# Kernel optimization log

Hardware: AMD Instinct MI355X
Metric: run time of the kernel (lower is better)

Reference implementation:

```python
import jax, jax.numpy as jnp
import numpy as np

B, A, D = 512, 32, 256      # batch clips, actors (nodes per graph), feature dim
E = 1048576                 # total edges over the flattened (B*A)-node graph
THRESHOLD = 0.5             # config.knn.threshold
EPS = 1e-5


def setup_inputs() -> dict:
    key = jax.random.key(0)
    k1, k2, k3 = jax.random.split(key, 3)
    N = B * A
    X = jax.random.normal(k1, (B, A, D), dtype=jnp.float32)
    edge_index = jax.random.randint(k2, (2, E), 0, N, dtype=jnp.int32)
    W = jax.random.normal(k3, (D, D), dtype=jnp.float32) * (1.0 / np.sqrt(D))
    b = jnp.zeros((D,), dtype=jnp.float32)
    return {"X": X, "edge_index": edge_index, "W": W, "b": b}


def gcn_conv(x, edge_index, W, b):
    # Standard GCNConv: x' = D^-1/2 (A + I) D^-1/2 (x W) + b
    N = x.shape[0]
    x = x @ W                                            # [N, D]
    loop = jnp.arange(N, dtype=edge_index.dtype)
    src = jnp.concatenate([edge_index[0], loop])         # message sources
    tgt = jnp.concatenate([edge_index[1], loop])         # aggregation targets
    deg = jax.ops.segment_sum(jnp.ones_like(src, dtype=x.dtype), tgt,
                              num_segments=N)            # in-degree incl. self-loop
    dinv = jnp.where(deg > 0, jax.lax.rsqrt(deg), 0.0)
    coef = (dinv[src] * dinv[tgt])[:, None]              # symmetric norm per edge
    out = jax.ops.segment_sum(x[src] * coef, tgt, num_segments=N)
    return out + b


def reference(X, edge_index, W, b):
    Bq, Aq, Dq = X.shape
    x = X.reshape(Bq * Aq, Dq)
    x = gcn_conv(x, edge_index, W, b)
    Xo = x.reshape(Bq, Aq, Dq)

    # cal_edge: pairwise squared distances per batch, min-max normalized,
    # thresholded. Instead of variable-length dense_to_sparse edge lists we
    # return the equivalent fixed-shape adjacency mask [B, A, A].
    inner = -2.0 * jnp.einsum('bad,bcd->bac', Xo, Xo)
    sq = jnp.sum(Xo * Xo, axis=-1, keepdims=True)        # [B, A, 1]
    scores = sq + inner + jnp.swapaxes(sq, -1, -2)       # [B, A, A]
    smin = scores.min(axis=-1, keepdims=True)
    smax = scores.max(axis=-1, keepdims=True)
    scores = (scores - smin) / (smax - smin + EPS)
    adj_mask = scores > THRESHOLD                        # new edge set (dense form)
    return Xo, adj_mask
```

## Files before the change

kernel.cpp:

```cpp
#include <hip/hip_runtime.h>

#define BQ 512
#define AQ 32
#define DQ 256
#define NQ (BQ * AQ)
#define EQ 1048576
#define THR 0.5f
#define EPSF 1e-5f
#define DEG_STRIDE 160
#define BIN_TGTS 64
#define NBINS (NQ / BIN_TGTS)
#define BIN_STRIDE 4864
#define HD 128

typedef __attribute__((ext_vector_type(8))) short bf16x8;
typedef __attribute__((ext_vector_type(4))) float f32x4;

__device__ __forceinline__ unsigned short f2bf(float f) {
    unsigned int u = __float_as_uint(f);
    return (unsigned short)((u + 0x7FFFu + ((u >> 16) & 1u)) >> 16);
}
__device__ __forceinline__ float bf2f(unsigned short h) {
    return __uint_as_float((unsigned int)h << 16);
}

__global__ __launch_bounds__(256) void k_prep_part(
        const float* __restrict__ W, unsigned short* __restrict__ Wt,
        const int* __restrict__ src, const int* __restrict__ tgt,
        int* __restrict__ bin_cursor, unsigned int* __restrict__ binned) {
    __shared__ int hist[NBINS];
    int tid = threadIdx.x;
    if (blockIdx.x < 256) {
        int idx = blockIdx.x * 256 + tid;
        int n = idx >> 8;
        int k = idx & 255;
        float w = W[k * DQ + n];
        unsigned short h = f2bf(w);
        Wt[idx] = h;
        Wt[DQ * DQ + idx] = f2bf(w - bf2f(h));
        return;
    }
    hist[tid] = 0;
    __syncthreads();
    int base = (blockIdx.x - 256) * 4096;
    int t[16], s[16];
    #pragma unroll
    for (int i = 0; i < 16; i++) {
        int e = base + i * 256 + tid;
        t[i] = tgt[e];
        s[i] = src[e];
        atomicAdd(&hist[t[i] >> 6], 1);
    }
    __syncthreads();
    int mine = hist[tid];
    __syncthreads();
    hist[tid] = tid * BIN_STRIDE + atomicAdd(&bin_cursor[tid], mine);
    __syncthreads();
    #pragma unroll
    for (int i = 0; i < 16; i++) {
        int slot = atomicAdd(&hist[t[i] >> 6], 1);
        binned[slot] = ((unsigned int)t[i] << 14) | (unsigned int)s[i];
    }
}

__global__ __launch_bounds__(256) void k_bucket_gemm(
        const float* __restrict__ Xp, const unsigned short* __restrict__ Wt,
        unsigned short* __restrict__ xwb,
        const int* __restrict__ bin_cursor, const unsigned int* __restrict__ binned,
        unsigned short* __restrict__ bucket, int* __restrict__ cnt) {
    __shared__ unsigned short lbuck[BIN_TGTS * DEG_STRIDE];
    __shared__ int lcnt[BIN_TGTS];
    int tid = threadIdx.x;
    if (blockIdx.x < NBINS) {
        int b = blockIdx.x;
        if (tid < BIN_TGTS) lcnt[tid] = 0;
        __syncthreads();
        int beg = b * BIN_STRIDE;
        int count = bin_cursor[b];
        if (count > BIN_STRIDE) count = BIN_STRIDE;
        int end = beg + count;
        for (int i = beg + tid; i < end; i += 256) {
            unsigned int ed = binned[i];
            int tl = (int)(ed >> 14) & 63;
            int pos = atomicAdd(&lcnt[tl], 1);
            if (pos < DEG_STRIDE)
                lbuck[tl * DEG_STRIDE + pos] = (unsigned short)(ed & 0x3FFFu);
        }
        __syncthreads();
        const unsigned int* lb32 = (const unsigned int*)lbuck;
        unsigned int* gb32 = (unsigned int*)(bucket + (size_t)b * BIN_TGTS * DEG_STRIDE);
        #pragma unroll
        for (int i = 0; i < 20; i++) gb32[i * 256 + tid] = lb32[i * 256 + tid];
        if (tid < BIN_TGTS) cnt[b * BIN_TGTS + tid] = lcnt[tid];
        return;
    }
    int wave = tid >> 6;
    int lane = tid & 63;
    int col = lane & 15;
    int quad = lane >> 4;
    int mbase = (blockIdx.x - NBINS) * 64 + wave * 16;
    int m = mbase + col;

    const float* arow = Xp + (size_t)m * DQ;
    const unsigned short* Wlo = Wt + DQ * DQ;

    f32x4 acc[16];
    f32x4 zero = {0.f, 0.f, 0.f, 0.f};
    #pragma unroll
    for (int i = 0; i < 16; i++) acc[i] = zero;

    for (int k0 = 0; k0 < DQ; k0 += 32) {
        int kq = k0 + quad * 8;
        float4 a0 = *(const float4*)(arow + kq);
        float4 a1 = *(const float4*)(arow + kq + 4);
        float av[8] = {a0.x, a0.y, a0.z, a0.w, a1.x, a1.y, a1.z, a1.w};
        bf16x8 ah, al;
        #pragma unroll
        for (int j = 0; j < 8; j++) {
            unsigned short h = f2bf(av[j]);
            ah[j] = (short)h;
            al[j] = (short)f2bf(av[j] - bf2f(h));
        }
        #pragma unroll
        for (int nt = 0; nt < 16; nt++) {
            size_t boff = (size_t)(nt * 16 + col) * DQ + kq;
            bf16x8 bh = *(const bf16x8*)(Wt + boff);
            bf16x8 bl = *(const bf16x8*)(Wlo + boff);
            acc[nt] = __builtin_amdgcn_mfma_f32_16x16x32_bf16(ah, bh, acc[nt], 0, 0, 0);
            acc[nt] = __builtin_amdgcn_mfma_f32_16x16x32_bf16(al, bh, acc[nt], 0, 0, 0);
            acc[nt] = __builtin_amdgcn_mfma_f32_16x16x32_bf16(ah, bl, acc[nt], 0, 0, 0);
        }
    }

    #pragma unroll
    for (int nt = 0; nt < 16; nt++) {
        int gc = nt * 16 + col;
        unsigned short* dst = xwb + (size_t)(gc >> 7) * NQ * HD;
        int c = gc & (HD - 1);
        #pragma unroll
        for (int r = 0; r < 4; r++) {
            dst[(size_t)(mbase + quad * 4 + r) * HD + c] = f2bf(acc[nt][r]);
        }
    }
}

__global__ __launch_bounds__(256) void k_agg(const unsigned int* __restrict__ xwb,
                                             const int* __restrict__ cnt,
                                             const unsigned short* __restrict__ bucket,
                                             const float* __restrict__ bias,
                                             float* __restrict__ out) {
    int wave = threadIdx.x >> 6;
    int lane = threadIdx.x & 63;
    int half = blockIdx.x >> 12;
    int t = (blockIdx.x & 4095) * 4 + wave;
    const unsigned int* plane = xwb + (size_t)half * NQ * (HD / 2);

    float dt = rsqrtf((float)(cnt[t] + 1));
    float c0 = dt * dt;
    unsigned int sp = plane[(size_t)t * 64 + lane];
    float2 acc;
    acc.x = __uint_as_float(sp << 16) * c0;
    acc.y = __uint_as_float(sp & 0xFFFF0000u) * c0;

    int beg = t * DEG_STRIDE;
    int num = cnt[t];
    if (num > DEG_STRIDE) num = DEG_STRIDE;
    for (int k0 = 0; k0 < num; k0 += 64) {
        int rem = num - k0;
        int n = rem < 64 ? rem : 64;
        int idx = beg + k0 + (lane < n ? lane : 0);
        int e = (int)bucket[idx];
        float cl = (lane < n) ? rsqrtf((float)(cnt[e] + 1)) * dt : 0.f;
        int n8 = (n + 7) & ~7;
        for (int j0 = 0; j0 < n8; j0 += 8) {
            #pragma unroll
            for (int jj = 0; jj < 8; jj++) {
                int j = j0 + jj;
                int s = __shfl(e, j);
                float c = __shfl(cl, j);
                unsigned int p = plane[(size_t)s * 64 + lane];
                acc.x += __uint_as_float(p << 16) * c;
                acc.y += __uint_as_float(p & 0xFFFF0000u) * c;
            }
        }
    }

    float2 bv = ((const float2*)bias)[half * 64 + lane];
    acc.x += bv.x; acc.y += bv.y;
    ((float2*)out)[(size_t)t * 128 + half * 64 + lane] = acc;
}

__global__ __launch_bounds__(256) void k_scores(const float* __restrict__ xo,
                                                float* __restrict__ mask) {
    __shared__ float xs[AQ][DQ + 4];
    __shared__ float sq[AQ];
    __shared__ float sc[AQ][AQ + 1];
    __shared__ float rmin[AQ], rmax[AQ];

    int bq = blockIdx.x;
    int tid = threadIdx.x;
    const float* xb = xo + (size_t)bq * AQ * DQ;

    for (int idx = tid; idx < AQ * DQ; idx += 256) {
        xs[idx >> 8][idx & 255] = xb[idx];
    }
    __syncthreads();

    if (tid < AQ) {
        const float4* xi = (const float4*)xs[tid];
        float s = 0.f;
        #pragma unroll 8
        for (int dd = 0; dd < DQ / 4; dd++) {
            float4 a = xi[dd];
            s += a.x * a.x + a.y * a.y + a.z * a.z + a.w * a.w;
        }
        sq[tid] = s;
    }
    __syncthreads();

    {
        int p0 = tid * 4;
        int i = p0 >> 5;
        int j0 = p0 & 31;
        const float4* xi = (const float4*)xs[i];
        float g[4] = {0.f, 0.f, 0.f, 0.f};
        for (int dd = 0; dd < DQ / 4; dd += 8) {
            float4 ar[8];
            #pragma unroll
            for (int u = 0; u < 8; u++) ar[u] = xi[dd + u];
            #pragma unroll
            for (int q = 0; q < 4; q++) {
                const float4* xj = (const float4*)xs[j0 + q];
                float gq = 0.f;
                #pragma unroll
                for (int u = 0; u < 8; u++) {
                    float4 b = xj[dd + u];
                    gq += ar[u].x * b.x + ar[u].y * b.y +
                          ar[u].z * b.z + ar[u].w * b.w;
                }
                g[q] += gq;
            }
        }
        #pragma unroll
        for (int q = 0; q < 4; q++) {
            sc[i][j0 + q] = sq[i] - 2.f * g[q] + sq[j0 + q];
        }
    }
    __syncthreads();

    if (tid < AQ) {
        float mn = sc[tid][0], mx = sc[tid][0];
        for (int j = 1; j < AQ; j++) {
            float v = sc[tid][j];
            mn = fminf(mn, v);
            mx = fmaxf(mx, v);
        }
        rmin[tid] = mn;
        rmax[tid] = mx;
    }
    __syncthreads();

    float* mb = mask + (size_t)bq * AQ * AQ;
    #pragma unroll
    for (int q = 0; q < 4; q++) {
        int p = tid * 4 + q;
        int i = p >> 5, j = p & 31;
        float v = (sc[i][j] - rmin[i]) / (rmax[i] - rmin[i] + EPSF);
        mb[p] = (v > THR) ? 1.0f : 0.0f;
    }
}

extern "C" void kernel_launch(void* const* d_in, const int* in_sizes, int n_in,
                              void* d_out, int out_size, void* d_ws, size_t ws_size,
                              hipStream_t stream) {
    const float* X    = (const float*)d_in[0];
    const int*   ei   = (const int*)d_in[1];
    const float* W    = (const float*)d_in[2];
    const float* bias = (const float*)d_in[3];
    float* out = (float*)d_out;

    char* ws = (char*)d_ws;
    unsigned short* xwb = (unsigned short*)ws;
    unsigned short* bucket = (unsigned short*)(ws + (size_t)NQ * DQ * 2);
    unsigned int* binned = (unsigned int*)(bucket + (size_t)NQ * DEG_STRIDE);
    unsigned short* Wt = (unsigned short*)(binned + (size_t)NBINS * BIN_STRIDE);
    int* cnt = (int*)(Wt + 2 * DQ * DQ);
    int* bin_cursor = cnt + NQ;

    const int* src = ei;
    const int* tgt = ei + EQ;

    hipMemsetAsync(bin_cursor, 0, NBINS * sizeof(int), stream);
    k_prep_part<<<512, 256, 0, stream>>>(W, Wt, src, tgt, bin_cursor, binned);
    k_bucket_gemm<<<512, 256, 0, stream>>>(X, Wt, xwb, bin_cursor, binned,
                                           bucket, cnt);
    k_agg<<<2 * NQ / 4, 256, 0, stream>>>((const unsigned int*)xwb, cnt, bucket,
                                          bias, out);
    k_scores<<<BQ, 256, 0, stream>>>(out, out + (size_t)NQ * DQ);
}
```

Baseline: 192.6 us.

## Precompute dinv and split aggregation wave into two half-waves with wider loads

The bucketing kernel now writes the per-node inverse square-root degree to a new dinv array, so the aggregation kernel reads it instead of recomputing rsqrt of counts. The aggregation kernel splits each wave into two 32-lane halves that process alternate edges, each lane loading uint2 (four bf16 values) instead of one uint. The halves are combined with a cross-half shuffle and written back with float4 stores. This removes the per-edge shuffles of indices and coefficients and raises the number of independent gathers in flight, at the cost of an extra workspace array and a final reduction.

```diff
diff --git a/kernel.cpp b/kernel.cpp
--- a/kernel.cpp
+++ b/kernel.cpp
@@ -67,7 +67,8 @@
         const float* __restrict__ Xp, const unsigned short* __restrict__ Wt,
         unsigned short* __restrict__ xwb,
         const int* __restrict__ bin_cursor, const unsigned int* __restrict__ binned,
-        unsigned short* __restrict__ bucket, int* __restrict__ cnt) {
+        unsigned short* __restrict__ bucket, int* __restrict__ cnt,
+        float* __restrict__ dinv) {
     __shared__ unsigned short lbuck[BIN_TGTS * DEG_STRIDE];
     __shared__ int lcnt[BIN_TGTS];
     int tid = threadIdx.x;
@@ -91,7 +92,11 @@
         unsigned int* gb32 = (unsigned int*)(bucket + (size_t)b * BIN_TGTS * DEG_STRIDE);
         #pragma unroll
         for (int i = 0; i < 20; i++) gb32[i * 256 + tid] = lb32[i * 256 + tid];
-        if (tid < BIN_TGTS) cnt[b * BIN_TGTS + tid] = lcnt[tid];
+        if (tid < BIN_TGTS) {
+            int c = lcnt[tid];
+            cnt[b * BIN_TGTS + tid] = c;
+            dinv[b * BIN_TGTS + tid] = rsqrtf((float)(c + 1));
+        }
         return;
     }
     int wave = tid >> 6;
@@ -147,47 +152,54 @@
 __global__ __launch_bounds__(256) void k_agg(const unsigned int* __restrict__ xwb,
                                              const int* __restrict__ cnt,
                                              const unsigned short* __restrict__ bucket,
+                                             const float* __restrict__ dinv,
                                              const float* __restrict__ bias,
                                              float* __restrict__ out) {
     int wave = threadIdx.x >> 6;
     int lane = threadIdx.x & 63;
+    int sub  = lane >> 5;
+    int sl   = lane & 31;
     int half = blockIdx.x >> 12;
     int t = (blockIdx.x & 4095) * 4 + wave;
-    const unsigned int* plane = xwb + (size_t)half * NQ * (HD / 2);
-
-    float dt = rsqrtf((float)(cnt[t] + 1));
-    float c0 = dt * dt;
-    unsigned int sp = plane[(size_t)t * 64 + lane];
-    float2 acc;
-    acc.x = __uint_as_float(sp << 16) * c0;
-    acc.y = __uint_as_float(sp & 0xFFFF0000u) * c0;
-
-    int beg = t * DEG_STRIDE;
+    const uint2* plane = (const uint2*)(xwb + (size_t)half * NQ * (HD / 2));
+
+    float dt = dinv[t];
+    float cself = sub ? 0.f : dt * dt;
+    uint2 sp = plane[(size_t)t * 32 + sl];
+    float4 acc;
+    acc.x = __uint_as_float(sp.x << 16) * cself;
+    acc.y = __uint_as_float(sp.x & 0xFFFF0000u) * cself;
+    acc.z = __uint_as_float(sp.y << 16) * cself;
+    acc.w = __uint_as_float(sp.y & 0xFFFF0000u) * cself;
+
+    const unsigned short* brow = bucket + t * DEG_STRIDE;
     int num = cnt[t];
     if (num > DEG_STRIDE) num = DEG_STRIDE;
-    for (int k0 = 0; k0 < num; k0 += 64) {
-        int rem = num - k0;
-        int n = rem < 64 ? rem : 64;
-        int idx = beg + k0 + (lane < n ? lane : 0);
-        int e = (int)bucket[idx];
-        float cl = (lane < n) ? rsqrtf((float)(cnt[e] + 1)) * dt : 0.f;
-        int n8 = (n + 7) & ~7;
-        for (int j0 = 0; j0 < n8; j0 += 8) {
-            #pragma unroll
-            for (int jj = 0; jj < 8; jj++) {
-                int j = j0 + jj;
-                int s = __shfl(e, j);
-                float c = __shfl(cl, j);
-                unsigned int p = plane[(size_t)s * 64 + lane];
-                acc.x += __uint_as_float(p << 16) * c;
-                acc.y += __uint_as_float(p & 0xFFFF0000u) * c;
-            }
-        }
-    }
-
-    float2 bv = ((const float2*)bias)[half * 64 + lane];
-    acc.x += bv.x; acc.y += bv.y;
-    ((float2*)out)[(size_t)t * 128 + half * 64 + lane] = acc;
+    for (int j0 = 0; j0 < num; j0 += 16) {
+        #pragma unroll
+        for (int jj = 0; jj < 16; jj += 2) {
+            int j = j0 + jj + sub;
+            int jv = j < num ? j : num - 1;
+            int e = (int)brow[jv];
+            float c = (j < num) ? dinv[e] * dt : 0.f;
+            uint2 p = plane[(size_t)e * 32 + sl];
+            acc.x += __uint_as_float(p.x << 16) * c;
+            acc.y += __uint_as_float(p.x & 0xFFFF0000u) * c;
+            acc.z += __uint_as_float(p.y << 16) * c;
+            acc.w += __uint_as_float(p.y & 0xFFFF0000u) * c;
+        }
+    }
+
+    acc.x += __shfl(acc.x, lane ^ 32);
+    acc.y += __shfl(acc.y, lane ^ 32);
+    acc.z += __shfl(acc.z, lane ^ 32);
+    acc.w += __shfl(acc.w, lane ^ 32);
+
+    if (sub == 0) {
+        float4 bv = ((const float4*)bias)[half * 32 + sl];
+        acc.x += bv.x; acc.y += bv.y; acc.z += bv.z; acc.w += bv.w;
+        ((float4*)out)[(size_t)t * 64 + half * 32 + sl] = acc;
+    }
 }
 
 __global__ __launch_bounds__(256) void k_scores(const float* __restrict__ xo,
@@ -285,7 +297,8 @@
     unsigned int* binned = (unsigned int*)(bucket + (size_t)NQ * DEG_STRIDE);
     unsigned short* Wt = (unsigned short*)(binned + (size_t)NBINS * BIN_STRIDE);
     int* cnt = (int*)(Wt + 2 * DQ * DQ);
-    int* bin_cursor = cnt + NQ;
+    float* dinv = (float*)(cnt + NQ);
+    int* bin_cursor = (int*)(dinv + NQ);
 
     const int* src = ei;
     const int* tgt = ei + EQ;
@@ -293,8 +306,8 @@
     hipMemsetAsync(bin_cursor, 0, NBINS * sizeof(int), stream);
     k_prep_part<<<512, 256, 0, stream>>>(W, Wt, src, tgt, bin_cursor, binned);
     k_bucket_gemm<<<512, 256, 0, stream>>>(X, Wt, xwb, bin_cursor, binned,
-                                           bucket, cnt);
+                                           bucket, cnt, dinv);
     k_agg<<<2 * NQ / 4, 256, 0, stream>>>((const unsigned int*)xwb, cnt, bucket,
-                                          bias, out);
+                                          dinv, bias, out);
     k_scores<<<BQ, 256, 0, stream>>>(out, out + (size_t)NQ * DQ);
 }
```

Measured after the change: 243.4 us. +26.4%, slower.
